# Kernel tuning notes

Hardware: AMD Instinct MI355X
Metric: run time of the kernel (lower is better)

Reference implementation:

```python
import jax, jax.numpy as jnp
import numpy as np

D_MODEL = 1024
NUM_HEADS = 16
D_HEAD = D_MODEL // NUM_HEADS
B, T = 2, 2048


def setup_inputs() -> dict:
    key = jax.random.key(0)
    kx, kq, kk, kv, ko = jax.random.split(key, 5)
    # xavier_uniform bound for square (D,D) linear weights
    bound = float(np.sqrt(6.0 / (D_MODEL + D_MODEL)))
    uni = lambda k: jax.random.uniform(k, (D_MODEL, D_MODEL), jnp.float32, -bound, bound)
    return {
        "x": jax.random.normal(kx, (B, T, D_MODEL), jnp.float32),
        "Wq": uni(kq),
        "Wk": uni(kk),
        "Wv": uni(kv),
        "Wo": uni(ko),
    }


def _split_heads(x):
    # (B, T, D) -> (B, H, T, d_head)
    b, t, _ = x.shape
    return x.reshape(b, t, NUM_HEADS, D_HEAD).transpose(0, 2, 1, 3)


def _exclusive_output_mod(Y, V):
    dt = V.dtype
    tiny = jnp.asarray(jnp.finfo(dt).tiny, dt)
    eps = jnp.asarray(jnp.finfo(dt).eps, dt)
    v_sq = jnp.sum(V * V, axis=-1, keepdims=True)
    y_dot_v = jnp.sum(Y * V, axis=-1, keepdims=True)
    scale = jnp.where(v_sq > 0, y_dot_v / jnp.maximum(v_sq, tiny), jnp.zeros_like(y_dot_v))
    Z = Y - scale * V
    residual_norm = jnp.linalg.norm(Z, axis=-1, keepdims=True)
    reference_norm = jnp.maximum(
        jnp.linalg.norm(Y, axis=-1, keepdims=True),
        jnp.linalg.norm(V, axis=-1, keepdims=True),
    )
    cleanup_tol = eps * Z.shape[-1] * reference_norm
    return jnp.where((v_sq > 0) & (residual_norm <= cleanup_tol), jnp.zeros_like(Z), Z)


def reference(x, Wq, Wk, Wv, Wo):
    Q = _split_heads(x @ Wq.T)  # (B,H,T,dh)
    K = _split_heads(x @ Wk.T)
    V = _split_heads(x @ Wv.T)
    sm_scale = 1.0 / np.sqrt(D_HEAD)
    scores = jnp.einsum("bhqd,bhkd->bhqk", Q, K) * sm_scale
    P = jax.nn.softmax(scores, axis=-1)
    Y = jnp.einsum("bhqk,bhkd->bhqd", P, V)
    Z = _exclusive_output_mod(Y, V)
    # merge heads: (B,H,T,dh) -> (B,T,D)
    Zm = Z.transpose(0, 2, 1, 3).reshape(x.shape[0], x.shape[1], D_MODEL)
    return Zm @ Wo.T
```

## Files before the change

### kernel.cpp

```cpp
#include <hip/hip_runtime.h>
#include <math.h>

#define DM   1024
#define TTOK 2048
#define NTOK 4096

typedef __bf16 bf16x8 __attribute__((ext_vector_type(8)));
typedef __bf16 bf16x4 __attribute__((ext_vector_type(4)));
typedef __bf16 bf16x2 __attribute__((ext_vector_type(2)));
typedef float  f32x4  __attribute__((ext_vector_type(4)));
typedef float  f32x16 __attribute__((ext_vector_type(16)));

#define QSCALE 0.18033688011112042f

#if defined(__has_builtin)
#if __has_builtin(__builtin_amdgcn_exp2f)
#define EXP2F(x) __builtin_amdgcn_exp2f(x)
#endif
#endif
#ifndef EXP2F
#define EXP2F(x) exp2f(x)
#endif

#define GLDS16(g, l) __builtin_amdgcn_global_load_lds( \
    (__attribute__((address_space(1))) void*)(g),      \
    (__attribute__((address_space(3))) void*)(l), 16, 0, 0)

__device__ __forceinline__ unsigned pk2(float a, float b) {
    bf16x2 t; t[0] = (__bf16)a; t[1] = (__bf16)b;
    return __builtin_bit_cast(unsigned, t);
}
union FU { unsigned u[4]; bf16x8 v; };

__global__ __launch_bounds__(256)
void cvt_all(const float* __restrict__ x,  const float* __restrict__ Wq,
             const float* __restrict__ Wk, const float* __restrict__ Wv,
             const float* __restrict__ Wo, __bf16* __restrict__ dst) {
    size_t g = ((size_t)blockIdx.x * 256 + threadIdx.x) * 8;
    const float* s;
    size_t off;
    const size_t NX = (size_t)NTOK * DM;
    if (g < NX) { s = x; off = g; }
    else {
        size_t gg = g - NX;
        int w = (int)(gg >> 20);
        off = gg & ((1u << 20) - 1);
        s = (w == 0) ? Wq : (w == 1) ? Wk : (w == 2) ? Wv : Wo;
    }
    float4 a = *(const float4*)(s + off);
    float4 b = *(const float4*)(s + off + 4);
    bf16x8 v;
    v[0] = (__bf16)a.x; v[1] = (__bf16)a.y; v[2] = (__bf16)a.z; v[3] = (__bf16)a.w;
    v[4] = (__bf16)b.x; v[5] = (__bf16)b.y; v[6] = (__bf16)b.z; v[7] = (__bf16)b.w;
    *(bf16x8*)(dst + g) = v;
}

#define LSTR 136
#define DBUF 8192

__global__ __launch_bounds__(256)
void gemm_qkv(const __bf16* __restrict__ X,
              const __bf16* __restrict__ W0, const __bf16* __restrict__ W1,
              const __bf16* __restrict__ W2,
              __bf16* __restrict__ Oq, __bf16* __restrict__ Ok,
              __bf16* __restrict__ Ovt)
{
    const int z = blockIdx.z;
    const __bf16 *A, *B;
    int m0, n0;
    if (z < 2) {
        A = z ? W1 : W0; B = X;
        m0 = blockIdx.y * 128; n0 = blockIdx.x * 128;
    } else {
        A = X; B = W2;
        m0 = blockIdx.x * 128; n0 = blockIdx.y * 128;
    }

    __shared__ __attribute__((aligned(16))) __bf16 smem[128 * LSTR];

    const int tid  = threadIdx.x;
    const int lane = tid & 63;
    const int wave = tid >> 6;
    const int wm = wave & 1, wn = wave >> 1;
    const int col = lane & 15, quad = lane >> 4;

    const __bf16* Ag = A + (size_t)(m0 + (tid >> 2)) * DM + (tid & 3) * 8;
    const __bf16* Bg = B + (size_t)(n0 + (tid >> 2)) * DM + (tid & 3) * 8;
    __bf16* lA = smem + tid * 8;
    __bf16* lB = smem + 4096 + tid * 8;

    f32x4 acc[4][4];
#pragma unroll
    for (int i = 0; i < 4; ++i)
#pragma unroll
        for (int j = 0; j < 4; ++j)
#pragma unroll
            for (int r = 0; r < 4; ++r) acc[i][j][r] = 0.0f;

    GLDS16(Ag,                   lA);
    GLDS16(Ag + (size_t)64 * DM, lA + 2048);
    GLDS16(Bg,                   lB);
    GLDS16(Bg + (size_t)64 * DM, lB + 2048);
    __syncthreads();

    const int nk = DM / 32;
    for (int t = 0; t < nk; ++t) {
        const int cur = (t & 1) * DBUF;
        const int nxt = DBUF - cur;

        if (t + 1 < nk) {
            const int k1 = (t + 1) * 32;
            GLDS16(Ag + k1,                   lA + nxt);
            GLDS16(Ag + (size_t)64 * DM + k1, lA + nxt + 2048);
            GLDS16(Bg + k1,                   lB + nxt);
            GLDS16(Bg + (size_t)64 * DM + k1, lB + nxt + 2048);
        }

        const __bf16* Asr = smem + cur;
        const __bf16* Bsr = smem + cur + 4096;
        bf16x8 af[4], bfr[4];
#pragma unroll
        for (int i = 0; i < 4; ++i)
            af[i] = *(const bf16x8*)&Asr[(wm * 64 + i * 16 + col) * 32 + quad * 8];
#pragma unroll
        for (int j = 0; j < 4; ++j)
            bfr[j] = *(const bf16x8*)&Bsr[(wn * 64 + j * 16 + col) * 32 + quad * 8];
#pragma unroll
        for (int i = 0; i < 4; ++i)
#pragma unroll
            for (int j = 0; j < 4; ++j)
                acc[i][j] = __builtin_amdgcn_mfma_f32_16x16x32_bf16(af[i], bfr[j], acc[i][j], 0, 0, 0);

        __syncthreads();
    }

    const float sc = (z == 0) ? QSCALE : 1.0f;
#pragma unroll
    for (int i = 0; i < 4; ++i)
#pragma unroll
        for (int j = 0; j < 4; ++j) {
            const int ml = wm * 64 + i * 16 + quad * 4;
            const int nl = wn * 64 + j * 16 + col;
            bf16x4 pk;
#pragma unroll
            for (int r = 0; r < 4; ++r) pk[r] = (__bf16)(acc[i][j][r] * sc);
            *(bf16x4*)&smem[nl * LSTR + ml] = pk;
        }
    __syncthreads();

#pragma unroll
    for (int it = 0; it < 8; ++it) {
        int c   = tid + 256 * it;
        int row = c >> 4;
        int ch  = (c & 15) * 8;
        bf16x8 v = *(const bf16x8*)&smem[row * LSTR + ch];
        if (z < 2) {
            int t  = n0 + row;
            int b  = t >> 11; t &= 2047;
            int hd = m0 + ch;
            int h  = hd >> 6, d = hd & 63;
            *(bf16x8*)&((z ? Ok : Oq)[(((size_t)(b * 16 + h)) * TTOK + t) * 64 + d]) = v;
        } else {
            int hd = n0 + row;
            int h  = hd >> 6, d = hd & 63;
            int t  = m0 + ch;
            int b  = t >> 11; t &= 2047;
            *(bf16x8*)&Ovt[(((size_t)(b * 16 + h)) * 64 + d) * TTOK + t] = v;
        }
    }
}

#define ODBUF 6144

__global__ __launch_bounds__(256)
void gemm_oproj(const __bf16* __restrict__ X, const __bf16* __restrict__ Wo,
                float* __restrict__ Of)
{
    const int f = blockIdx.x + 8 * blockIdx.y;
    const int c = f & 7, i0 = f >> 3;
    const int m0 = (8 * c + (i0 & 7)) * 64;
    const int n0 = (i0 >> 3) * 128;

    __shared__ __attribute__((aligned(16))) __bf16 smem[2 * ODBUF];

    const int tid  = threadIdx.x;
    const int lane = tid & 63;
    const int wave = tid >> 6;
    const int col = lane & 15, quad = lane >> 4;

    const __bf16* Ag = X  + (size_t)(m0 + (tid >> 2)) * DM + (tid & 3) * 8;
    const __bf16* Bg = Wo + (size_t)(n0 + (tid >> 2)) * DM + (tid & 3) * 8;
    __bf16* lA = smem + tid * 8;
    __bf16* lB = smem + 2048 + tid * 8;

    f32x4 acc[4][2];
#pragma unroll
    for (int i = 0; i < 4; ++i)
#pragma unroll
        for (int j = 0; j < 2; ++j)
#pragma unroll
            for (int r = 0; r < 4; ++r) acc[i][j][r] = 0.0f;

    GLDS16(Ag,                   lA);
    GLDS16(Bg,                   lB);
    GLDS16(Bg + (size_t)64 * DM, lB + 2048);
    __syncthreads();

    const int nk = DM / 32;
    for (int t = 0; t < nk; ++t) {
        const int cur = (t & 1) * ODBUF;
        const int nxt = ODBUF - cur;
        if (t + 1 < nk) {
            const int k1 = (t + 1) * 32;
            GLDS16(Ag + k1,                   lA + nxt);
            GLDS16(Bg + k1,                   lB + nxt);
            GLDS16(Bg + (size_t)64 * DM + k1, lB + nxt + 2048);
        }
        const __bf16* Asr = smem + cur;
        const __bf16* Bsr = smem + cur + 2048;
        bf16x8 af[4], bfr[2];
#pragma unroll
        for (int i = 0; i < 4; ++i)
            af[i] = *(const bf16x8*)&Asr[(i * 16 + col) * 32 + quad * 8];
#pragma unroll
        for (int j = 0; j < 2; ++j)
            bfr[j] = *(const bf16x8*)&Bsr[(wave * 32 + j * 16 + col) * 32 + quad * 8];
#pragma unroll
        for (int i = 0; i < 4; ++i)
#pragma unroll
            for (int j = 0; j < 2; ++j)
                acc[i][j] = __builtin_amdgcn_mfma_f32_16x16x32_bf16(af[i], bfr[j], acc[i][j], 0, 0, 0);
        __syncthreads();
    }

#pragma unroll
    for (int i = 0; i < 4; ++i)
#pragma unroll
        for (int j = 0; j < 2; ++j) {
            const int mb = m0 + i * 16 + quad * 4;
            const int n  = n0 + wave * 32 + j * 16 + col;
#pragma unroll
            for (int r = 0; r < 4; ++r)
                Of[(size_t)(mb + r) * DM + n] = acc[i][j][r];
        }
}

__global__ __launch_bounds__(512, 4)
void attn_mfma(const __bf16* __restrict__ Qg, const __bf16* __restrict__ Kg,
               const __bf16* __restrict__ Vtg, __bf16* __restrict__ Zm)
{
    const int bh = blockIdx.y;
    const int q0 = blockIdx.x * 128;
    const size_t base = (size_t)bh * TTOK * 64;

    __shared__ __attribute__((aligned(16))) __bf16 lds[2][2][2][64 * 72];

    const int tid  = threadIdx.x;
    const int lane = tid & 63;
    const int wave = tid >> 6;
    const int half = wave >> 2;
    const int qw   = wave & 3;
    const int c32  = lane & 31, h32 = lane >> 5;

    bf16x8 qf[4];
    const __bf16* qrow = Qg + base + (size_t)(q0 + qw * 32 + c32) * 64 + h32 * 8;
#pragma unroll
    for (int st = 0; st < 4; ++st)
        qf[st] = *(const bf16x8*)(qrow + st * 16);

    f32x16 O[2];
#pragma unroll
    for (int r = 0; r < 16; ++r) { O[0][r] = 0.0f; O[1][r] = 0.0f; }
    float lsum = 0.0f;

    const int tid8 = tid & 255;
    const int rs   = tid8 >> 2;
    const int soff = (tid8 & 3) * 16;
    const int kb0  = half * 1024;

    {
        const __bf16* kp = Kg  + base + (size_t)(kb0 + rs) * 64 + soff;
        const __bf16* vp = Vtg + base + (size_t)rs * TTOK + kb0 + soff;
        bf16x8 k0 = *(const bf16x8*)(kp);
        bf16x8 k1 = *(const bf16x8*)(kp + 8);
        bf16x8 v0 = *(const bf16x8*)(vp);
        bf16x8 v1 = *(const bf16x8*)(vp + 8);
        *(bf16x8*)&lds[half][0][0][rs * 72 + soff]     = k0;
        *(bf16x8*)&lds[half][0][0][rs * 72 + soff + 8] = k1;
        *(bf16x8*)&lds[half][1][0][rs * 72 + soff]     = v0;
        *(bf16x8*)&lds[half][1][0][rs * 72 + soff + 8] = v1;
    }
    bf16x8 kr0, kr1, vr0, vr1;
    {
        const __bf16* kp = Kg  + base + (size_t)(kb0 + 64 + rs) * 64 + soff;
        const __bf16* vp = Vtg + base + (size_t)rs * TTOK + kb0 + 64 + soff;
        kr0 = *(const bf16x8*)(kp); kr1 = *(const bf16x8*)(kp + 8);
        vr0 = *(const bf16x8*)(vp); vr1 = *(const bf16x8*)(vp + 8);
    }
    __syncthreads();

    for (int it = 0; it < 16; ++it) {
        const int cur = it & 1;
        const __bf16* Kc = &lds[half][0][cur][0];
        const __bf16* Vc = &lds[half][1][cur][0];

        f32x16 s0, s1;
#pragma unroll
        for (int r = 0; r < 16; ++r) { s0[r] = 0.0f; s1[r] = 0.0f; }
#pragma unroll
        for (int st = 0; st < 4; ++st) {
            bf16x8 a0 = *(const bf16x8*)&Kc[(c32)      * 72 + h32 * 8 + st * 16];
            bf16x8 a1 = *(const bf16x8*)&Kc[(32 + c32) * 72 + h32 * 8 + st * 16];
            s0 = __builtin_amdgcn_mfma_f32_32x32x16_bf16(a0, qf[st], s0, 0, 0, 0);
            s1 = __builtin_amdgcn_mfma_f32_32x32x16_bf16(a1, qf[st], s1, 0, 0, 0);
        }

#pragma unroll
        for (int ks = 0; ks < 4; ++ks) {
            const f32x16& sv = (ks & 2) ? s1 : s0;
            const int rb = (ks & 1) * 8;
            float p0 = EXP2F(sv[rb + 0]), p1 = EXP2F(sv[rb + 1]);
            float p2 = EXP2F(sv[rb + 2]), p3 = EXP2F(sv[rb + 3]);
            float p4 = EXP2F(sv[rb + 4]), p5 = EXP2F(sv[rb + 5]);
            float p6 = EXP2F(sv[rb + 6]), p7 = EXP2F(sv[rb + 7]);
            lsum += ((p0 + p1) + (p2 + p3)) + ((p4 + p5) + (p6 + p7));
            unsigned A0 = pk2(p0, p1), A1 = pk2(p2, p3);
            unsigned B0 = pk2(p4, p5), B1 = pk2(p6, p7);
            unsigned s0w = h32 ? A0 : B0;
            unsigned s1w = h32 ? A1 : B1;
            unsigned r0 = __shfl_xor(s0w, 32, 64);
            unsigned r1 = __shfl_xor(s1w, 32, 64);
            FU fu;
            fu.u[0] = h32 ? r0 : A0;
            fu.u[1] = h32 ? r1 : A1;
            fu.u[2] = h32 ? B0 : r0;
            fu.u[3] = h32 ? B1 : r1;
            bf16x8 v0 = *(const bf16x8*)&Vc[(c32)      * 72 + h32 * 8 + ks * 16];
            bf16x8 v1 = *(const bf16x8*)&Vc[(32 + c32) * 72 + h32 * 8 + ks * 16];
            O[0] = __builtin_amdgcn_mfma_f32_32x32x16_bf16(v0, fu.v, O[0], 0, 0, 0);
            O[1] = __builtin_amdgcn_mfma_f32_32x32x16_bf16(v1, fu.v, O[1], 0, 0, 0);
        }

        *(bf16x8*)&lds[half][0][cur ^ 1][rs * 72 + soff]     = kr0;
        *(bf16x8*)&lds[half][0][cur ^ 1][rs * 72 + soff + 8] = kr1;
        *(bf16x8*)&lds[half][1][cur ^ 1][rs * 72 + soff]     = vr0;
        *(bf16x8*)&lds[half][1][cur ^ 1][rs * 72 + soff + 8] = vr1;

        {
            int itn = (it + 2) & 15;
            const __bf16* kp = Kg  + base + (size_t)(kb0 + itn * 64 + rs) * 64 + soff;
            const __bf16* vp = Vtg + base + (size_t)rs * TTOK + kb0 + itn * 64 + soff;
            kr0 = *(const bf16x8*)(kp); kr1 = *(const bf16x8*)(kp + 8);
            vr0 = *(const bf16x8*)(vp); vr1 = *(const bf16x8*)(vp + 8);
        }

        __syncthreads();
    }

    float* cb = (float*)&lds[0][0][0][0];
    if (wave >= 4) {
        float* me = cb + qw * 2048 + lane * 32;
#pragma unroll
        for (int r = 0; r < 16; ++r) { me[r] = O[0][r]; me[16 + r] = O[1][r]; }
        cb[8192 + qw * 64 + lane] = lsum;
    }
    __syncthreads();
    if (wave >= 4) return;
    {
        const float* pr = cb + qw * 2048 + lane * 32;
#pragma unroll
        for (int r = 0; r < 16; ++r) { O[0][r] += pr[r]; O[1][r] += pr[16 + r]; }
        lsum += cb[8192 + qw * 64 + lane];
    }
    const float ltot = lsum + __shfl_xor(lsum, 32, 64);
    const float inv  = 1.0f / ltot;

    const int q = q0 + qw * 32 + c32;
    float vq[2][16];
#pragma unroll
    for (int db = 0; db < 2; ++db)
#pragma unroll
        for (int rg = 0; rg < 16; ++rg) {
            int d = db * 32 + (rg & 3) + 8 * (rg >> 2) + 4 * h32;
            vq[db][rg] = (float)Vtg[base + (size_t)d * TTOK + q];
        }

    const int b = bh >> 4, h = bh & 15;
    float y[2][16];
    float yv = 0.f, v2 = 0.f, yy = 0.f;
#pragma unroll
    for (int db = 0; db < 2; ++db)
#pragma unroll
        for (int rg = 0; rg < 16; ++rg) {
            float yval = O[db][rg] * inv;
            float vval = vq[db][rg];
            y[db][rg] = yval;
            yv += yval * vval; v2 += vval * vval; yy += yval * yval;
        }
    yv += __shfl_xor(yv, 32, 64);
    v2 += __shfl_xor(v2, 32, 64);
    yy += __shfl_xor(yy, 32, 64);
    float scl = (v2 > 0.0f) ? yv / fmaxf(v2, 1.1754943508222875e-38f) : 0.0f;
    float zz = 0.f;
    float zvv[2][16];
#pragma unroll
    for (int db = 0; db < 2; ++db)
#pragma unroll
        for (int rg = 0; rg < 16; ++rg) {
            zvv[db][rg] = y[db][rg] - scl * vq[db][rg];
            zz += zvv[db][rg] * zvv[db][rg];
        }
    zz += __shfl_xor(zz, 32, 64);
    float znorm = sqrtf(zz);
    float refn  = fmaxf(sqrtf(yy), sqrtf(v2));
    bool  wipe  = (v2 > 0.0f) && (znorm <= 1.1920928955078125e-07f * 64.0f * refn);
#pragma unroll
    for (int db = 0; db < 2; ++db)
#pragma unroll
        for (int g = 0; g < 4; ++g) {
            bf16x4 pk;
#pragma unroll
            for (int r = 0; r < 4; ++r)
                pk[r] = (__bf16)(wipe ? 0.0f : zvv[db][4 * g + r]);
            int d = db * 32 + 8 * g + 4 * h32;
            *(bf16x4*)&Zm[((size_t)(b * TTOK + q)) * DM + h * 64 + d] = pk;
        }
}

extern "C" void kernel_launch(void* const* d_in, const int* in_sizes, int n_in,
                              void* d_out, int out_size, void* d_ws, size_t ws_size,
                              hipStream_t stream) {
    const float* x  = (const float*)d_in[0];
    const float* Wq = (const float*)d_in[1];
    const float* Wk = (const float*)d_in[2];
    const float* Wv = (const float*)d_in[3];
    const float* Wo = (const float*)d_in[4];

    const size_t NX = (size_t)NTOK * DM;
    const size_t NW = (size_t)DM * DM;
    __bf16* xb  = (__bf16*)d_ws;
    __bf16* wqb = xb  + NX;
    __bf16* wkb = wqb + NW;
    __bf16* wvb = wkb + NW;
    __bf16* wob = wvb + NW;
    __bf16* Qb  = wob + NW;
    __bf16* Kb  = Qb  + NX;
    __bf16* Vtb = Kb  + NX;
    __bf16* Zmb = Vtb + NX;

    cvt_all<<<(NX + 4 * NW) / 2048, 256, 0, stream>>>(x, Wq, Wk, Wv, Wo, xb);

    gemm_qkv<<<dim3(32, 8, 3), 256, 0, stream>>>(
        xb, wqb, wkb, wvb, Qb, Kb, Vtb);

    attn_mfma<<<dim3(TTOK / 128, 32), 512, 0, stream>>>(Qb, Kb, Vtb, Zmb);

    gemm_oproj<<<dim3(8, 64), 256, 0, stream>>>(Zmb, wob, (float*)d_out);
}
```

Baseline: 184.6 us.

## Halve attention block to 4 waves, each wave computing two 32-row query tiles

The attention kernel now runs 256 threads per block instead of 512. Each wave owns 64 query rows (two 32-row sub-tiles) rather than 32, so every K and V fragment read from LDS feeds twice as many MFMAs. Each thread now loads four K/V vectors per stage instead of two. The aim is to cut LDS traffic per unit of work and raise MFMA density per wave, at the cost of doubling the accumulator and score registers, which may lower occupancy. The cross-half reduction is also relaid out so the shared buffer is indexed by lane.

```diff
diff --git a/kernel.cpp b/kernel.cpp
--- a/kernel.cpp
+++ b/kernel.cpp
@@ -245,7 +245,7 @@
         }
 }
 
-__global__ __launch_bounds__(512, 4)
+__global__ __launch_bounds__(256)
 void attn_mfma(const __bf16* __restrict__ Qg, const __bf16* __restrict__ Kg,
                const __bf16* __restrict__ Vtg, __bf16* __restrict__ Zm)
 {
@@ -258,44 +258,58 @@
     const int tid  = threadIdx.x;
     const int lane = tid & 63;
     const int wave = tid >> 6;
-    const int half = wave >> 2;
-    const int qw   = wave & 3;
+    const int p    = wave & 1;
+    const int half = wave >> 1;
     const int c32  = lane & 31, h32 = lane >> 5;
 
-    bf16x8 qf[4];
-    const __bf16* qrow = Qg + base + (size_t)(q0 + qw * 32 + c32) * 64 + h32 * 8;
-#pragma unroll
-    for (int st = 0; st < 4; ++st)
-        qf[st] = *(const bf16x8*)(qrow + st * 16);
-
-    f32x16 O[2];
-#pragma unroll
-    for (int r = 0; r < 16; ++r) { O[0][r] = 0.0f; O[1][r] = 0.0f; }
-    float lsum = 0.0f;
-
-    const int tid8 = tid & 255;
-    const int rs   = tid8 >> 2;
-    const int soff = (tid8 & 3) * 16;
-    const int kb0  = half * 1024;
+    bf16x8 qf[2][4];
+#pragma unroll
+    for (int qs = 0; qs < 2; ++qs) {
+        const __bf16* qrow = Qg + base
+            + (size_t)(q0 + p * 64 + qs * 32 + c32) * 64 + h32 * 8;
+#pragma unroll
+        for (int st = 0; st < 4; ++st)
+            qf[qs][st] = *(const bf16x8*)(qrow + st * 16);
+    }
+
+    f32x16 O[2][2];
+#pragma unroll
+    for (int qs = 0; qs < 2; ++qs)
+#pragma unroll
+        for (int db = 0; db < 2; ++db)
+#pragma unroll
+            for (int r = 0; r < 16; ++r) O[qs][db][r] = 0.0f;
+    float lsum[2] = {0.0f, 0.0f};
+
+    const int tid128 = tid & 127;
+    const int rs  = tid128 >> 2;
+    const int eo  = (tid128 & 3) * 16;
+    const int kb0 = half * 1024;
 
     {
-        const __bf16* kp = Kg  + base + (size_t)(kb0 + rs) * 64 + soff;
-        const __bf16* vp = Vtg + base + (size_t)rs * TTOK + kb0 + soff;
-        bf16x8 k0 = *(const bf16x8*)(kp);
-        bf16x8 k1 = *(const bf16x8*)(kp + 8);
-        bf16x8 v0 = *(const bf16x8*)(vp);
-        bf16x8 v1 = *(const bf16x8*)(vp + 8);
-        *(bf16x8*)&lds[half][0][0][rs * 72 + soff]     = k0;
-        *(bf16x8*)&lds[half][0][0][rs * 72 + soff + 8] = k1;
-        *(bf16x8*)&lds[half][1][0][rs * 72 + soff]     = v0;
-        *(bf16x8*)&lds[half][1][0][rs * 72 + soff + 8] = v1;
-    }
-    bf16x8 kr0, kr1, vr0, vr1;
+        const __bf16* kp = Kg  + base + (size_t)(kb0 + rs) * 64 + eo;
+        const __bf16* vp = Vtg + base + (size_t)rs * TTOK + kb0 + eo;
+        *(bf16x8*)&lds[half][0][0][rs * 72 + eo]            = *(const bf16x8*)(kp);
+        *(bf16x8*)&lds[half][0][0][rs * 72 + eo + 8]        = *(const bf16x8*)(kp + 8);
+        *(bf16x8*)&lds[half][0][0][(rs + 32) * 72 + eo]     = *(const bf16x8*)(kp + (size_t)32 * 64);
+        *(bf16x8*)&lds[half][0][0][(rs + 32) * 72 + eo + 8] = *(const bf16x8*)(kp + (size_t)32 * 64 + 8);
+        *(bf16x8*)&lds[half][1][0][rs * 72 + eo]            = *(const bf16x8*)(vp);
+        *(bf16x8*)&lds[half][1][0][rs * 72 + eo + 8]        = *(const bf16x8*)(vp + 8);
+        *(bf16x8*)&lds[half][1][0][(rs + 32) * 72 + eo]     = *(const bf16x8*)(vp + (size_t)32 * TTOK);
+        *(bf16x8*)&lds[half][1][0][(rs + 32) * 72 + eo + 8] = *(const bf16x8*)(vp + (size_t)32 * TTOK + 8);
+    }
+    bf16x8 kr[4], vr[4];
     {
-        const __bf16* kp = Kg  + base + (size_t)(kb0 + 64 + rs) * 64 + soff;
-        const __bf16* vp = Vtg + base + (size_t)rs * TTOK + kb0 + 64 + soff;
-        kr0 = *(const bf16x8*)(kp); kr1 = *(const bf16x8*)(kp + 8);
-        vr0 = *(const bf16x8*)(vp); vr1 = *(const bf16x8*)(vp + 8);
+        const __bf16* kp = Kg  + base + (size_t)(kb0 + 64 + rs) * 64 + eo;
+        const __bf16* vp = Vtg + base + (size_t)rs * TTOK + kb0 + 64 + eo;
+        kr[0] = *(const bf16x8*)(kp);
+        kr[1] = *(const bf16x8*)(kp + 8);
+        kr[2] = *(const bf16x8*)(kp + (size_t)32 * 64);
+        kr[3] = *(const bf16x8*)(kp + (size_t)32 * 64 + 8);
+        vr[0] = *(const bf16x8*)(vp);
+        vr[1] = *(const bf16x8*)(vp + 8);
+        vr[2] = *(const bf16x8*)(vp + (size_t)32 * TTOK);
+        vr[3] = *(const bf16x8*)(vp + (size_t)32 * TTOK + 8);
     }
     __syncthreads();
 
@@ -304,127 +318,174 @@
         const __bf16* Kc = &lds[half][0][cur][0];
         const __bf16* Vc = &lds[half][1][cur][0];
 
-        f32x16 s0, s1;
-#pragma unroll
-        for (int r = 0; r < 16; ++r) { s0[r] = 0.0f; s1[r] = 0.0f; }
+        f32x16 s[2][2];
+#pragma unroll
+        for (int qs = 0; qs < 2; ++qs)
+#pragma unroll
+            for (int rh = 0; rh < 2; ++rh)
+#pragma unroll
+                for (int r = 0; r < 16; ++r) s[qs][rh][r] = 0.0f;
 #pragma unroll
         for (int st = 0; st < 4; ++st) {
             bf16x8 a0 = *(const bf16x8*)&Kc[(c32)      * 72 + h32 * 8 + st * 16];
             bf16x8 a1 = *(const bf16x8*)&Kc[(32 + c32) * 72 + h32 * 8 + st * 16];
-            s0 = __builtin_amdgcn_mfma_f32_32x32x16_bf16(a0, qf[st], s0, 0, 0, 0);
-            s1 = __builtin_amdgcn_mfma_f32_32x32x16_bf16(a1, qf[st], s1, 0, 0, 0);
+#pragma unroll
+            for (int qs = 0; qs < 2; ++qs) {
+                s[qs][0] = __builtin_amdgcn_mfma_f32_32x32x16_bf16(a0, qf[qs][st], s[qs][0], 0, 0, 0);
+                s[qs][1] = __builtin_amdgcn_mfma_f32_32x32x16_bf16(a1, qf[qs][st], s[qs][1], 0, 0, 0);
+            }
+        }
+
+        bf16x8 pf[2][4];
+#pragma unroll
+        for (int qs = 0; qs < 2; ++qs) {
+#pragma unroll
+            for (int ks = 0; ks < 4; ++ks) {
+                const f32x16& sv = (ks & 2) ? s[qs][1] : s[qs][0];
+                const int rb = (ks & 1) * 8;
+                float p0 = EXP2F(sv[rb + 0]), p1 = EXP2F(sv[rb + 1]);
+                float p2 = EXP2F(sv[rb + 2]), p3 = EXP2F(sv[rb + 3]);
+                float p4 = EXP2F(sv[rb + 4]), p5 = EXP2F(sv[rb + 5]);
+                float p6 = EXP2F(sv[rb + 6]), p7 = EXP2F(sv[rb + 7]);
+                lsum[qs] += ((p0 + p1) + (p2 + p3)) + ((p4 + p5) + (p6 + p7));
+                unsigned A0 = pk2(p0, p1), A1 = pk2(p2, p3);
+                unsigned B0 = pk2(p4, p5), B1 = pk2(p6, p7);
+                unsigned s0w = h32 ? A0 : B0;
+                unsigned s1w = h32 ? A1 : B1;
+                unsigned r0 = __shfl_xor(s0w, 32, 64);
+                unsigned r1 = __shfl_xor(s1w, 32, 64);
+                FU fu;
+                fu.u[0] = h32 ? r0 : A0;
+                fu.u[1] = h32 ? r1 : A1;
+                fu.u[2] = h32 ? B0 : r0;
+                fu.u[3] = h32 ? B1 : r1;
+                pf[qs][ks] = fu.v;
+            }
         }
 
 #pragma unroll
         for (int ks = 0; ks < 4; ++ks) {
-            const f32x16& sv = (ks & 2) ? s1 : s0;
-            const int rb = (ks & 1) * 8;
-            float p0 = EXP2F(sv[rb + 0]), p1 = EXP2F(sv[rb + 1]);
-            float p2 = EXP2F(sv[rb + 2]), p3 = EXP2F(sv[rb + 3]);
-            float p4 = EXP2F(sv[rb + 4]), p5 = EXP2F(sv[rb + 5]);
-            float p6 = EXP2F(sv[rb + 6]), p7 = EXP2F(sv[rb + 7]);
-            lsum += ((p0 + p1) + (p2 + p3)) + ((p4 + p5) + (p6 + p7));
-            unsigned A0 = pk2(p0, p1), A1 = pk2(p2, p3);
-            unsigned B0 = pk2(p4, p5), B1 = pk2(p6, p7);
-            unsigned s0w = h32 ? A0 : B0;
-            unsigned s1w = h32 ? A1 : B1;
-            unsigned r0 = __shfl_xor(s0w, 32, 64);
-            unsigned r1 = __shfl_xor(s1w, 32, 64);
-            FU fu;
-            fu.u[0] = h32 ? r0 : A0;
-            fu.u[1] = h32 ? r1 : A1;
-            fu.u[2] = h32 ? B0 : r0;
-            fu.u[3] = h32 ? B1 : r1;
             bf16x8 v0 = *(const bf16x8*)&Vc[(c32)      * 72 + h32 * 8 + ks * 16];
             bf16x8 v1 = *(const bf16x8*)&Vc[(32 + c32) * 72 + h32 * 8 + ks * 16];
-            O[0] = __builtin_amdgcn_mfma_f32_32x32x16_bf16(v0, fu.v, O[0], 0, 0, 0);
-            O[1] = __builtin_amdgcn_mfma_f32_32x32x16_bf16(v1, fu.v, O[1], 0, 0, 0);
-        }
-
-        *(bf16x8*)&lds[half][0][cur ^ 1][rs * 72 + soff]     = kr0;
-        *(bf16x8*)&lds[half][0][cur ^ 1][rs * 72 + soff + 8] = kr1;
-        *(bf16x8*)&lds[half][1][cur ^ 1][rs * 72 + soff]     = vr0;
-        *(bf16x8*)&lds[half][1][cur ^ 1][rs * 72 + soff + 8] = vr1;
+#pragma unroll
+            for (int qs = 0; qs < 2; ++qs) {
+                O[qs][0] = __builtin_amdgcn_mfma_f32_32x32x16_bf16(v0, pf[qs][ks], O[qs][0], 0, 0, 0);
+                O[qs][1] = __builtin_amdgcn_mfma_f32_32x32x16_bf16(v1, pf[qs][ks], O[qs][1], 0, 0, 0);
+            }
+        }
+
+        {
+            __bf16* Kn = &lds[half][0][cur ^ 1][0];
+            __bf16* Vn = &lds[half][1][cur ^ 1][0];
+            *(bf16x8*)&Kn[rs * 72 + eo]            = kr[0];
+            *(bf16x8*)&Kn[rs * 72 + eo + 8]        = kr[1];
+            *(bf16x8*)&Kn[(rs + 32) * 72 + eo]     = kr[2];
+            *(bf16x8*)&Kn[(rs + 32) * 72 + eo + 8] = kr[3];
+            *(bf16x8*)&Vn[rs * 72 + eo]            = vr[0];
+            *(bf16x8*)&Vn[rs * 72 + eo + 8]        = vr[1];
+            *(bf16x8*)&Vn[(rs + 32) * 72 + eo]     = vr[2];
+            *(bf16x8*)&Vn[(rs + 32) * 72 + eo + 8] = vr[3];
+        }
 
         {
             int itn = (it + 2) & 15;
-            const __bf16* kp = Kg  + base + (size_t)(kb0 + itn * 64 + rs) * 64 + soff;
-            const __bf16* vp = Vtg + base + (size_t)rs * TTOK + kb0 + itn * 64 + soff;
-            kr0 = *(const bf16x8*)(kp); kr1 = *(const bf16x8*)(kp + 8);
-            vr0 = *(const bf16x8*)(vp); vr1 = *(const bf16x8*)(vp + 8);
+            const __bf16* kp = Kg  + base + (size_t)(kb0 + itn * 64 + rs) * 64 + eo;
+            const __bf16* vp = Vtg + base + (size_t)rs * TTOK + kb0 + itn * 64 + eo;
+            kr[0] = *(const bf16x8*)(kp);
+            kr[1] = *(const bf16x8*)(kp + 8);
+            kr[2] = *(const bf16x8*)(kp + (size_t)32 * 64);
+            kr[3] = *(const bf16x8*)(kp + (size_t)32 * 64 + 8);
+            vr[0] = *(const bf16x8*)(vp);
+            vr[1] = *(const bf16x8*)(vp + 8);
+            vr[2] = *(const bf16x8*)(vp + (size_t)32 * TTOK);
+            vr[3] = *(const bf16x8*)(vp + (size_t)32 * TTOK + 8);
         }
 
         __syncthreads();
     }
 
     float* cb = (float*)&lds[0][0][0][0];
-    if (wave >= 4) {
-        float* me = cb + qw * 2048 + lane * 32;
-#pragma unroll
-        for (int r = 0; r < 16; ++r) { me[r] = O[0][r]; me[16 + r] = O[1][r]; }
-        cb[8192 + qw * 64 + lane] = lsum;
+    if (half == 1) {
+#pragma unroll
+        for (int qs = 0; qs < 2; ++qs) {
+            float* me = cb + (p * 2 + qs) * 2048;
+#pragma unroll
+            for (int db = 0; db < 2; ++db)
+#pragma unroll
+                for (int r = 0; r < 16; ++r)
+                    me[(db * 16 + r) * 64 + lane] = O[qs][db][r];
+            cb[8192 + (p * 2 + qs) * 64 + lane] = lsum[qs];
+        }
     }
     __syncthreads();
-    if (wave >= 4) return;
-    {
-        const float* pr = cb + qw * 2048 + lane * 32;
-#pragma unroll
-        for (int r = 0; r < 16; ++r) { O[0][r] += pr[r]; O[1][r] += pr[16 + r]; }
-        lsum += cb[8192 + qw * 64 + lane];
-    }
-    const float ltot = lsum + __shfl_xor(lsum, 32, 64);
-    const float inv  = 1.0f / ltot;
-
-    const int q = q0 + qw * 32 + c32;
-    float vq[2][16];
-#pragma unroll
-    for (int db = 0; db < 2; ++db)
-#pragma unroll
-        for (int rg = 0; rg < 16; ++rg) {
-            int d = db * 32 + (rg & 3) + 8 * (rg >> 2) + 4 * h32;
-            vq[db][rg] = (float)Vtg[base + (size_t)d * TTOK + q];
-        }
+    if (half == 1) return;
+#pragma unroll
+    for (int qs = 0; qs < 2; ++qs) {
+        const float* pr = cb + (p * 2 + qs) * 2048;
+#pragma unroll
+        for (int db = 0; db < 2; ++db)
+#pragma unroll
+            for (int r = 0; r < 16; ++r)
+                O[qs][db][r] += pr[(db * 16 + r) * 64 + lane];
+        lsum[qs] += cb[8192 + (p * 2 + qs) * 64 + lane];
+    }
 
     const int b = bh >> 4, h = bh & 15;
-    float y[2][16];
-    float yv = 0.f, v2 = 0.f, yy = 0.f;
-#pragma unroll
-    for (int db = 0; db < 2; ++db)
-#pragma unroll
-        for (int rg = 0; rg < 16; ++rg) {
-            float yval = O[db][rg] * inv;
-            float vval = vq[db][rg];
-            y[db][rg] = yval;
-            yv += yval * vval; v2 += vval * vval; yy += yval * yval;
-        }
-    yv += __shfl_xor(yv, 32, 64);
-    v2 += __shfl_xor(v2, 32, 64);
-    yy += __shfl_xor(yy, 32, 64);
-    float scl = (v2 > 0.0f) ? yv / fmaxf(v2, 1.1754943508222875e-38f) : 0.0f;
-    float zz = 0.f;
-    float zvv[2][16];
-#pragma unroll
-    for (int db = 0; db < 2; ++db)
-#pragma unroll
-        for (int rg = 0; rg < 16; ++rg) {
-            zvv[db][rg] = y[db][rg] - scl * vq[db][rg];
-            zz += zvv[db][rg] * zvv[db][rg];
-        }
-    zz += __shfl_xor(zz, 32, 64);
-    float znorm = sqrtf(zz);
-    float refn  = fmaxf(sqrtf(yy), sqrtf(v2));
-    bool  wipe  = (v2 > 0.0f) && (znorm <= 1.1920928955078125e-07f * 64.0f * refn);
-#pragma unroll
-    for (int db = 0; db < 2; ++db)
-#pragma unroll
-        for (int g = 0; g < 4; ++g) {
-            bf16x4 pk;
-#pragma unroll
-            for (int r = 0; r < 4; ++r)
-                pk[r] = (__bf16)(wipe ? 0.0f : zvv[db][4 * g + r]);
-            int d = db * 32 + 8 * g + 4 * h32;
-            *(bf16x4*)&Zm[((size_t)(b * TTOK + q)) * DM + h * 64 + d] = pk;
-        }
+#pragma unroll
+    for (int qs = 0; qs < 2; ++qs) {
+        const float ltot = lsum[qs] + __shfl_xor(lsum[qs], 32, 64);
+        const float inv  = 1.0f / ltot;
+        const int q = q0 + p * 64 + qs * 32 + c32;
+
+        float vq[2][16];
+#pragma unroll
+        for (int db = 0; db < 2; ++db)
+#pragma unroll
+            for (int rg = 0; rg < 16; ++rg) {
+                int d = db * 32 + (rg & 3) + 8 * (rg >> 2) + 4 * h32;
+                vq[db][rg] = (float)Vtg[base + (size_t)d * TTOK + q];
+            }
+
+        float y[2][16];
+        float yv = 0.f, v2 = 0.f, yy = 0.f;
+#pragma unroll
+        for (int db = 0; db < 2; ++db)
+#pragma unroll
+            for (int rg = 0; rg < 16; ++rg) {
+                float yval = O[qs][db][rg] * inv;
+                float vval = vq[db][rg];
+                y[db][rg] = yval;
+                yv += yval * vval; v2 += vval * vval; yy += yval * yval;
+            }
+        yv += __shfl_xor(yv, 32, 64);
+        v2 += __shfl_xor(v2, 32, 64);
+        yy += __shfl_xor(yy, 32, 64);
+        float scl = (v2 > 0.0f) ? yv / fmaxf(v2, 1.1754943508222875e-38f) : 0.0f;
+        float zz = 0.f;
+        float zvv[2][16];
+#pragma unroll
+        for (int db = 0; db < 2; ++db)
+#pragma unroll
+            for (int rg = 0; rg < 16; ++rg) {
+                zvv[db][rg] = y[db][rg] - scl * vq[db][rg];
+                zz += zvv[db][rg] * zvv[db][rg];
+            }
+        zz += __shfl_xor(zz, 32, 64);
+        float znorm = sqrtf(zz);
+        float refn  = fmaxf(sqrtf(yy), sqrtf(v2));
+        bool  wipe  = (v2 > 0.0f) && (znorm <= 1.1920928955078125e-07f * 64.0f * refn);
+#pragma unroll
+        for (int db = 0; db < 2; ++db)
+#pragma unroll
+            for (int g = 0; g < 4; ++g) {
+                bf16x4 pk;
+#pragma unroll
+                for (int r = 0; r < 4; ++r)
+                    pk[r] = (__bf16)(wipe ? 0.0f : zvv[db][4 * g + r]);
+                int d = db * 32 + 8 * g + 4 * h32;
+                *(bf16x4*)&Zm[((size_t)(b * TTOK + q)) * DM + h * 64 + d] = pk;
+            }
+    }
 }
 
 extern "C" void kernel_launch(void* const* d_in, const int* in_sizes, int n_in,
@@ -453,7 +514,7 @@
     gemm_qkv<<<dim3(32, 8, 3), 256, 0, stream>>>(
         xb, wqb, wkb, wvb, Qb, Kb, Vtb);
 
-    attn_mfma<<<dim3(TTOK / 128, 32), 512, 0, stream>>>(Qb, Kb, Vtb, Zmb);
+    attn_mfma<<<dim3(TTOK / 128, 32), 256, 0, stream>>>(Qb, Kb, Vtb, Zmb);
 
     gemm_oproj<<<dim3(8, 64), 256, 0, stream>>>(Zmb, wob, (float*)d_out);
 }
```

Result: slower. 196.0 us (+6.2%).
